# Kernel optimization log

Measured on AMD Instinct MI355X. Metric: run time of the kernel, lower is better.

## Reference

```python
import jax, jax.numpy as jnp
import numpy as np

D_MODEL = 1024
NUM_HEADS = 16
D_K = D_MODEL // NUM_HEADS
THETA = 10000.0
BATCH, SEQ = 2, 2048


def apply_rope(x, token_positions, theta):
    # x: [..., heads, seq, d_k]; interleaved pair rotation
    d = x.shape[-1]
    inv_freq = theta ** (-jnp.arange(0, d, 2, dtype=jnp.float32) / d)  # [d/2]
    ang = token_positions.astype(jnp.float32)[:, None] * inv_freq[None, :]  # [seq, d/2]
    cos, sin = jnp.cos(ang), jnp.sin(ang)  # broadcast over batch/heads
    x_even = x[..., 0::2]
    x_odd = x[..., 1::2]
    out_even = x_even * cos - x_odd * sin
    out_odd = x_even * sin + x_odd * cos
    out = jnp.stack([out_even, out_odd], axis=-1)  # [..., seq, d/2, 2]
    return out.reshape(x.shape)


def setup_inputs() -> dict:
    key = jax.random.key(0)
    ks = jax.random.split(key, 5)
    scale = 1.0 / np.sqrt(D_MODEL)
    return {
        "x": jax.random.normal(ks[0], (BATCH, SEQ, D_MODEL), dtype=jnp.float32),
        "wq": jax.random.normal(ks[1], (D_MODEL, D_MODEL), dtype=jnp.float32) * scale,
        "wk": jax.random.normal(ks[2], (D_MODEL, D_MODEL), dtype=jnp.float32) * scale,
        "wv": jax.random.normal(ks[3], (D_MODEL, D_MODEL), dtype=jnp.float32) * scale,
        "wo": jax.random.normal(ks[4], (D_MODEL, D_MODEL), dtype=jnp.float32) * scale,
        "token_positions": jnp.arange(SEQ, dtype=jnp.int32),
    }


def reference(x, wq, wk, wv, wo, token_positions):
    B, S, _ = x.shape
    # fused-style QKV projections: weight layout is [d_out, d_in]
    xq = jnp.einsum("bsd,kd->bsk", x, wq)
    xk = jnp.einsum("bsd,kd->bsk", x, wk)
    xv = jnp.einsum("bsd,vd->bsv", x, wv)
    # split heads: [b, h, s, d_h]
    def split(t):
        return t.reshape(B, S, NUM_HEADS, D_K).transpose(0, 2, 1, 3)
    xq, xk, xv = split(xq), split(xk), split(xv)
    xq = apply_rope(xq, token_positions, THETA)
    xk = apply_rope(xk, token_positions, THETA)
    scores = jnp.einsum("bhqd,bhkd->bhqk", xq, xk) / jnp.sqrt(jnp.float32(D_K))
    causal = jnp.tril(jnp.ones((S, S), dtype=bool))
    scores = jnp.where(causal, scores, -jnp.inf)
    attn = jax.nn.softmax(scores, axis=-1)
    out = jnp.einsum("bhqk,bhkd->bhqd", attn, xv)
    out = out.transpose(0, 2, 1, 3).reshape(B, S, D_MODEL)  # merge heads
    return jnp.einsum("bsv,dv->bsd", out, wo)
```

## Files before the change

kernel.cpp:

```cpp
#include <hip/hip_runtime.h>

typedef __attribute__((ext_vector_type(8))) short short8;
typedef __attribute__((ext_vector_type(4))) short short4v;
typedef __attribute__((ext_vector_type(4))) float floatx4;

__device__ inline ushort f2b(float f) {
    union { uint i; float f; } c; c.f = f;
    uint i = c.i;
    uint r = (i + 0x7FFFu + ((i >> 16) & 1u)) >> 16;
    return (ushort)r;
}

__device__ __forceinline__ void load_lds16(const ushort* g, ushort* l) {
    __builtin_amdgcn_global_load_lds((const __attribute__((address_space(1))) void*)g,
                                     (__attribute__((address_space(3))) void*)l, 16, 0, 0);
}

__global__ __launch_bounds__(256) void cvt4_k(const float* __restrict__ x,
                                              const float* __restrict__ wq,
                                              const float* __restrict__ wk,
                                              const float* __restrict__ wv,
                                              ushort* __restrict__ xb,
                                              ushort* __restrict__ wqb,
                                              ushort* __restrict__ wkb,
                                              ushort* __restrict__ wvb,
                                              const int* __restrict__ pos,
                                              float2* __restrict__ tab) {
    const int blk = blockIdx.x;
    if (blk >= 3584) {
        const int idx = (blk - 3584) * 256 + threadIdx.x;
        const int s = idx >> 5, fi = idx & 31;
        const float inv = exp2f(-(float)fi * 0.41524101186092557f);
        const float ang = (float)pos[s] * inv;
        float sn, cs;
        sincosf(ang, &sn, &cs);
        tab[idx] = make_float2(cs, sn);
        return;
    }
    const float* in; ushort* out; int base;
    if (blk < 2048)      { in = x;  out = xb;  base = blk; }
    else if (blk < 2560) { in = wq; out = wqb; base = blk - 2048; }
    else if (blk < 3072) { in = wk; out = wkb; base = blk - 2560; }
    else                 { in = wv; out = wvb; base = blk - 3072; }
    const int i = (base * 256 + threadIdx.x) * 8;
    float4 f0 = *(const float4*)(in + i);
    float4 f1 = *(const float4*)(in + i + 4);
    ushort u[8] = {f2b(f0.x), f2b(f0.y), f2b(f0.z), f2b(f0.w),
                   f2b(f1.x), f2b(f1.y), f2b(f1.z), f2b(f1.w)};
    *(uint4*)(out + i) = *(const uint4*)u;
}

__global__ __launch_bounds__(256) void cvt_k(const float* __restrict__ in,
                                             ushort* __restrict__ out, int n) {
    const int i = (blockIdx.x * 256 + threadIdx.x) * 8;
    if (i >= n) return;
    float4 f0 = *(const float4*)(in + i);
    float4 f1 = *(const float4*)(in + i + 4);
    ushort u[8] = {f2b(f0.x), f2b(f0.y), f2b(f0.z), f2b(f0.w),
                   f2b(f1.x), f2b(f1.y), f2b(f1.z), f2b(f1.w)};
    *(uint4*)(out + i) = *(const uint4*)u;
}

template <bool OUTF32>
__device__ __forceinline__ void gemm_body8(ushort* As, ushort* Bs,
                                           const ushort* __restrict__ A,
                                           const ushort* __restrict__ B,
                                           void* __restrict__ C,
                                           int N, int m0, int n0,
                                           bool doRope, const float2* __restrict__ tab,
                                           float oscale) {
    const int tid = threadIdx.x;
    const int wave = tid >> 6, lane = tid & 63;
    const int quad = lane >> 4, l16 = lane & 15;
    const int wm = (wave >> 2) * 64, wn = (wave & 3) * 32;

    floatx4 acc[4][2] = {};

    const int rA = tid >> 2, jgA = ((tid & 3) - (rA >> 1)) & 3;
    const ushort* ga = A + (size_t)(m0 + rA) * 1024 + jgA * 8;
    const ushort* gb = B + (size_t)(n0 + rA) * 1024 + jgA * 8;

    load_lds16(ga, As + tid * 8);
    load_lds16(gb, Bs + tid * 8);
    __syncthreads();

    for (int kt = 0; kt < 32; ++kt) {
        const int cur = kt & 1;
        if (kt + 1 < 32) {
            const int nb = (cur ^ 1) * 4096;
            load_lds16(ga + (kt + 1) * 32, As + nb + tid * 8);
            load_lds16(gb + (kt + 1) * 32, Bs + nb + tid * 8);
        }
        const ushort* as = As + cur * 4096;
        const ushort* bs = Bs + cur * 4096;
        short8 af[4], bf[2];
#pragma unroll
        for (int i = 0; i < 4; ++i) {
            const int ra = wm + i * 16 + l16;
            af[i] = *(const short8*)(as + ra * 32 + (((quad + (ra >> 1)) & 3) << 3));
        }
#pragma unroll
        for (int j = 0; j < 2; ++j) {
            const int rb = wn + j * 16 + l16;
            bf[j] = *(const short8*)(bs + rb * 32 + (((quad + (rb >> 1)) & 3) << 3));
        }
#pragma unroll
        for (int mi = 0; mi < 4; ++mi)
#pragma unroll
            for (int ni = 0; ni < 2; ++ni)
                acc[mi][ni] = __builtin_amdgcn_mfma_f32_16x16x32_bf16(af[mi], bf[ni], acc[mi][ni], 0, 0, 0);
        __syncthreads();
    }
#pragma unroll
    for (int mi = 0; mi < 4; ++mi) {
        const int row = m0 + wm + mi * 16 + quad * 4;
#pragma unroll
        for (int ni = 0; ni < 2; ++ni) {
            const int col = n0 + wn + ni * 16 + l16;
            const int fi = ((wn + ni * 16 + l16) & 63) >> 1;
#pragma unroll
            for (int r = 0; r < 4; ++r) {
                float v = acc[mi][ni][r];
                if (doRope) {
                    const float other = __shfl_xor(v, 1);
                    const float2 cs = tab[((row + r) & 2047) * 32 + fi];
                    v = (col & 1) ? (other * cs.y + v * cs.x) : (v * cs.x - other * cs.y);
                }
                v *= oscale;
                if (OUTF32) ((float*)C)[(size_t)(row + r) * N + col] = v;
                else        ((ushort*)C)[(size_t)(row + r) * N + col] = f2b(v);
            }
        }
    }
}

__global__ __launch_bounds__(512) void gemm_qkv(const ushort* __restrict__ xb,
                                                const ushort* __restrict__ wqb,
                                                const ushort* __restrict__ wkb,
                                                const ushort* __restrict__ wvb,
                                                ushort* __restrict__ q,
                                                ushort* __restrict__ k,
                                                ushort* __restrict__ vt,
                                                const float2* __restrict__ tab) {
    __shared__ __align__(16) ushort As[8192], Bs[8192];
    const int blk = blockIdx.x;
    const int job = blk >> 8, r = blk & 255;
    const ushort *A, *B;
    ushort* C;
    int N, m0, n0;
    bool rope;
    float osc;
    if (job == 0)      { A = xb;  B = wqb; C = q;  N = 1024; m0 = (r >> 3) * 128; n0 = (r & 7) * 128; rope = true;  osc = 0.18033688011112042f; }
    else if (job == 1) { A = xb;  B = wkb; C = k;  N = 1024; m0 = (r >> 3) * 128; n0 = (r & 7) * 128; rope = true;  osc = 1.0f; }
    else               { A = wvb; B = xb;  C = vt; N = 4096; m0 = (r & 7) * 128;  n0 = (r >> 3) * 128; rope = false; osc = 1.0f; }
    gemm_body8<false>(As, Bs, A, B, C, N, m0, n0, rope, tab, osc);
}

__global__ __launch_bounds__(512) void gemm_o(const ushort* __restrict__ A,
                                              const ushort* __restrict__ B,
                                              float* __restrict__ C) {
    __shared__ __align__(16) ushort As[8192];
    __shared__ __align__(16) ushort Bs[4096];

    const int blk = blockIdx.x;
    const int m0 = (blk >> 4) * 128, n0 = (blk & 15) * 64;

    const int tid = threadIdx.x;
    const int wave = tid >> 6, lane = tid & 63;
    const int quad = lane >> 4, l16 = lane & 15;
    const int wm = (wave >> 2) * 64, wn = (wave & 3) * 16;

    floatx4 acc[4] = {};

    const int rA = tid >> 2, jgA = ((tid & 3) - (rA >> 1)) & 3;
    const ushort* ga = A + (size_t)(m0 + rA) * 1024 + jgA * 8;
    const int rB = (tid & 255) >> 2, jgB = (((tid & 255) & 3) - (rB >> 1)) & 3;
    const ushort* gb = B + (size_t)(n0 + rB) * 1024 + jgB * 8;

    load_lds16(ga, As + tid * 8);
    if (tid < 256) load_lds16(gb, Bs + tid * 8);
    __syncthreads();

    for (int kt = 0; kt < 32; ++kt) {
        const int cur = kt & 1;
        if (kt + 1 < 32) {
            load_lds16(ga + (kt + 1) * 32, As + (cur ^ 1) * 4096 + tid * 8);
            if (tid < 256)
                load_lds16(gb + (kt + 1) * 32, Bs + (cur ^ 1) * 2048 + tid * 8);
        }
        const ushort* as = As + cur * 4096;
        const ushort* bs = Bs + cur * 2048;
        short8 af[4], bf;
#pragma unroll
        for (int i = 0; i < 4; ++i) {
            const int ra = wm + i * 16 + l16;
            af[i] = *(const short8*)(as + ra * 32 + (((quad + (ra >> 1)) & 3) << 3));
        }
        {
            const int rb = wn + l16;
            bf = *(const short8*)(bs + rb * 32 + (((quad + (rb >> 1)) & 3) << 3));
        }
#pragma unroll
        for (int mi = 0; mi < 4; ++mi)
            acc[mi] = __builtin_amdgcn_mfma_f32_16x16x32_bf16(af[mi], bf, acc[mi], 0, 0, 0);
        __syncthreads();
    }
#pragma unroll
    for (int mi = 0; mi < 4; ++mi) {
        const int row = m0 + wm + mi * 16 + quad * 4;
        const int col = n0 + wn + l16;
#pragma unroll
        for (int r = 0; r < 4; ++r)
            C[(size_t)(row + r) * 1024 + col] = acc[mi][r];
    }
}

__global__ __launch_bounds__(256, 4) void attn_k(const ushort* __restrict__ Qg,
                                                 const ushort* __restrict__ Kg,
                                                 const ushort* __restrict__ Vtg,
                                                 ushort* __restrict__ Og,
                                                 const float* __restrict__ wo,
                                                 ushort* __restrict__ wob) {
    __shared__ __align__(16) ushort Ks[2][4096];
    __shared__ __align__(16) ushort Vs[2][4096];

    const int tid = threadIdx.x;
    const int blk = blockIdx.x;
    if (blk >= 1024) {
        const int i = ((blk - 1024) * 256 + tid) * 8;
        float4 f0 = *(const float4*)(wo + i);
        float4 f1 = *(const float4*)(wo + i + 4);
        ushort u[8] = {f2b(f0.x), f2b(f0.y), f2b(f0.z), f2b(f0.w),
                       f2b(f1.x), f2b(f1.y), f2b(f1.z), f2b(f1.w)};
        *(uint4*)(wob + i) = *(const uint4*)u;
        return;
    }
    const int wave = tid >> 6, lane = tid & 63;
    const int quad = lane >> 4, l16 = lane & 15;
    const int g = blk >> 8, rem = blk & 255;
    const int t = rem >> 5, bh = rem & 31;
    int qt;
    if (g == 0)      qt = 31 - t;
    else if (g == 1) qt = 23 - t;
    else if (g == 2) qt = t;
    else             qt = 8 + t;
    const int b = bh >> 4, h = bh & 15;
    const int bq = b * 2048;
    const int wl = wave * 16 + l16;
    const int nk = qt + 1, dt = nk - 1;

    const int cA = tid, cB = tid + 256;
    const int sA = cA >> 3, jA = ((cA & 7) - sA) & 7;
    const int sB = cB >> 3, jB = ((cB & 7) - sB) & 7;
    const ushort* kgA = Kg + (size_t)(bq + sA) * 1024 + h * 64 + jA * 8;
    const ushort* kgB = Kg + (size_t)(bq + sB) * 1024 + h * 64 + jB * 8;
    const ushort* vgA = Vtg + (size_t)(h * 64 + sA) * 4096 + bq + jA * 8;
    const ushort* vgB = Vtg + (size_t)(h * 64 + sB) * 4096 + bq + jB * 8;

    const int kb0 = l16 * 64 + (((quad + l16) & 7) << 3);
    const int kb1 = l16 * 64 + (((quad + 4 + l16) & 7) << 3);
    int vbs[4];
#pragma unroll
    for (int cb = 0; cb < 4; ++cb)
        vbs[cb] = l16 * 64 + (((cb * 2 + (quad >> 1) + l16) & 7) << 3) + (quad & 1) * 4;

    const ushort* qrow = Qg + (size_t)(bq + qt * 64 + wl) * 1024 + h * 64 + quad * 8;
    const short8 qf0 = *(const short8*)qrow;
    const short8 qf1 = *(const short8*)(qrow + 32);

    floatx4 od[4] = {};
    float l_st = 0.0f;

    load_lds16(kgA, &Ks[0][cA * 8]);
    load_lds16(kgB, &Ks[0][cB * 8]);
    load_lds16(vgA, &Vs[0][cA * 8]);
    load_lds16(vgB, &Vs[0][cB * 8]);
    __syncthreads();

    const ushort* kgA2 = kgA + 65536;
    const ushort* kgB2 = kgB + 65536;
    const ushort* vgA2 = vgA + 64;
    const ushort* vgB2 = vgB + 64;

    auto step = [&](int kt, bool diag, bool pref) {
        const int cur = kt & 1;
        if (pref) {
            const int nxt = cur ^ 1;
            load_lds16(kgA2, &Ks[nxt][cA * 8]);
            load_lds16(kgB2, &Ks[nxt][cB * 8]);
            load_lds16(vgA2, &Vs[nxt][cA * 8]);
            load_lds16(vgB2, &Vs[nxt][cB * 8]);
            kgA2 += 65536; kgB2 += 65536; vgA2 += 64; vgB2 += 64;
        }
        const ushort* kc = &Ks[cur][0];
        const ushort* vc = &Vs[cur][0];

        floatx4 st[4];
        __builtin_amdgcn_s_setprio(1);
#pragma unroll
        for (int cb = 0; cb < 4; ++cb) {
            short8 kf0 = *(const short8*)(kc + kb0 + cb * 1024);
            short8 kf1 = *(const short8*)(kc + kb1 + cb * 1024);
            floatx4 z = {};
            z = __builtin_amdgcn_mfma_f32_16x16x32_bf16(kf0, qf0, z, 0, 0, 0);
            z = __builtin_amdgcn_mfma_f32_16x16x32_bf16(kf1, qf1, z, 0, 0, 0);
            st[cb] = z;
        }
        __builtin_amdgcn_s_setprio(0);

        float pv[4][4];
        float sum = 0.0f;
#pragma unroll
        for (int cb = 0; cb < 4; ++cb) {
            const int scb = cb * 16 + quad * 4;
#pragma unroll
            for (int r = 0; r < 4; ++r) {
                float e = __builtin_amdgcn_exp2f(st[cb][r]);
                if (diag && (scb + r > wl)) e = 0.0f;
                pv[cb][r] = e;
                sum += e;
            }
        }
        l_st += sum;

        short4v pb[4];
#pragma unroll
        for (int cb = 0; cb < 4; ++cb) {
            uint lo_, hi_;
            asm("v_cvt_pk_bf16_f32 %0, %1, %2" : "=v"(lo_) : "v"(pv[cb][0]), "v"(pv[cb][1]));
            asm("v_cvt_pk_bf16_f32 %0, %1, %2" : "=v"(hi_) : "v"(pv[cb][2]), "v"(pv[cb][3]));
            union { uint u[2]; short4v s; } cvu;
            cvu.u[0] = lo_; cvu.u[1] = hi_;
            pb[cb] = cvu.s;
        }

        __builtin_amdgcn_s_setprio(1);
#pragma unroll
        for (int db = 0; db < 4; ++db) {
#pragma unroll
            for (int cb = 0; cb < 4; ++cb) {
                short4v vf = *(const short4v*)(vc + vbs[cb] + db * 1024);
                od[db] = __builtin_amdgcn_mfma_f32_16x16x16bf16_1k(vf, pb[cb], od[db], 0, 0, 0);
            }
        }
        __builtin_amdgcn_s_setprio(0);
        if (pref) __syncthreads();
    };

    for (int kt = 0; kt < dt; ++kt) step(kt, false, true);
    step(dt, true, false);

    l_st += __shfl_xor(l_st, 16);
    l_st += __shfl_xor(l_st, 32);

    const float linv = 1.0f / l_st;
    ushort* orow = Og + (size_t)(bq + qt * 64 + wl) * 1024 + h * 64 + quad * 4;
#pragma unroll
    for (int db = 0; db < 4; ++db) {
        uint2 w;
        w.x = (uint)f2b(od[db][0] * linv) | ((uint)f2b(od[db][1] * linv) << 16);
        w.y = (uint)f2b(od[db][2] * linv) | ((uint)f2b(od[db][3] * linv) << 16);
        *(uint2*)(orow + db * 16) = w;
    }
}

extern "C" void kernel_launch(void* const* d_in, const int* in_sizes, int n_in,
                              void* d_out, int out_size, void* d_ws, size_t ws_size,
                              hipStream_t stream) {
    const float* x  = (const float*)d_in[0];
    const float* wq = (const float*)d_in[1];
    const float* wk = (const float*)d_in[2];
    const float* wv = (const float*)d_in[3];
    const float* wo = (const float*)d_in[4];
    const int* pos  = (const int*)d_in[5];

    const size_t NX = (size_t)4096 * 1024;
    const size_t NW = (size_t)1024 * 1024;

    ushort* q_ws  = (ushort*)d_ws;
    ushort* k_ws  = q_ws + NX;
    ushort* vt_ws = k_ws + NX;
    ushort* o_ws  = vt_ws + NX;
    ushort* xb  = (ushort*)d_out;
    ushort* wqb = xb + NX;
    ushort* wkb = wqb + NW;
    ushort* wvb = wkb + NW;
    float2* tab = (float2*)(wvb + NW);

    const bool merged = ws_size >= (4 * NX + NW) * sizeof(ushort);
    ushort* wob = merged ? (o_ws + NX) : q_ws;

    cvt4_k<<<dim3(3840), 256, 0, stream>>>(x, wq, wk, wv, xb, wqb, wkb, wvb, pos, tab);
    gemm_qkv<<<dim3(768), 512, 0, stream>>>(xb, wqb, wkb, wvb, q_ws, k_ws, vt_ws, tab);
    attn_k<<<dim3(merged ? 1536 : 1024), 256, 0, stream>>>(q_ws, k_ws, vt_ws, o_ws, wo, wob);
    if (!merged)
        cvt_k<<<dim3(512), 256, 0, stream>>>(wo, q_ws, (int)NW);
    gemm_o<<<dim3(512), 512, 0, stream>>>(o_ws, wob, (float*)d_out);
}
```

Baseline: 179.4 us.

## Pair complementary causal query tiles in one 512-thread attention block sharing K/V loads

The attention kernel now packs two query tiles into one 8-wave block: one half takes a late tile (qt=31-j) and the other an early tile (qt=j). Both halves share the same staged K/V tiles in LDS, so the early tile's K/V loads are reused and every block does balanced causal work. The cost is that half the waves sit idle (still hitting barriers) once the short tile finishes, and there are fewer, larger blocks with different occupancy.

```diff
diff --git a/kernel.cpp b/kernel.cpp
--- a/kernel.cpp
+++ b/kernel.cpp
@@ -215,7 +215,7 @@
     }
 }
 
-__global__ __launch_bounds__(256, 4) void attn_k(const ushort* __restrict__ Qg,
+__global__ __launch_bounds__(512, 4) void attn_k(const ushort* __restrict__ Qg,
                                                  const ushort* __restrict__ Kg,
                                                  const ushort* __restrict__ Vtg,
                                                  ushort* __restrict__ Og,
@@ -226,8 +226,8 @@
 
     const int tid = threadIdx.x;
     const int blk = blockIdx.x;
-    if (blk >= 1024) {
-        const int i = ((blk - 1024) * 256 + tid) * 8;
+    if (blk >= 512) {
+        const int i = ((blk - 512) * 512 + tid) * 8;
         float4 f0 = *(const float4*)(wo + i);
         float4 f1 = *(const float4*)(wo + i + 4);
         ushort u[8] = {f2b(f0.x), f2b(f0.y), f2b(f0.z), f2b(f0.w),
@@ -237,25 +237,21 @@
     }
     const int wave = tid >> 6, lane = tid & 63;
     const int quad = lane >> 4, l16 = lane & 15;
-    const int g = blk >> 8, rem = blk & 255;
-    const int t = rem >> 5, bh = rem & 31;
-    int qt;
-    if (g == 0)      qt = 31 - t;
-    else if (g == 1) qt = 23 - t;
-    else if (g == 2) qt = t;
-    else             qt = 8 + t;
+    const int half = wave >> 2, wv = wave & 3;
+    const int bh = blk & 31;
+    const int t = blk >> 5;
+    const int jIdx = (t < 8) ? t : (23 - t);
+    const int qt = half ? jIdx : (31 - jIdx);
+    const int nkA = 32 - jIdx;
+    const int nkB = jIdx + 1;
+    const int nk = half ? nkB : nkA;
     const int b = bh >> 4, h = bh & 15;
     const int bq = b * 2048;
-    const int wl = wave * 16 + l16;
-    const int nk = qt + 1, dt = nk - 1;
-
-    const int cA = tid, cB = tid + 256;
-    const int sA = cA >> 3, jA = ((cA & 7) - sA) & 7;
-    const int sB = cB >> 3, jB = ((cB & 7) - sB) & 7;
-    const ushort* kgA = Kg + (size_t)(bq + sA) * 1024 + h * 64 + jA * 8;
-    const ushort* kgB = Kg + (size_t)(bq + sB) * 1024 + h * 64 + jB * 8;
-    const ushort* vgA = Vtg + (size_t)(h * 64 + sA) * 4096 + bq + jA * 8;
-    const ushort* vgB = Vtg + (size_t)(h * 64 + sB) * 4096 + bq + jB * 8;
+    const int wl = wv * 16 + l16;
+
+    const int sK = tid >> 3, jK = ((tid & 7) - sK) & 7;
+    const ushort* kg = Kg + (size_t)(bq + sK) * 1024 + h * 64 + jK * 8;
+    const ushort* vg = Vtg + (size_t)(h * 64 + sK) * 4096 + bq + jK * 8;
 
     const int kb0 = l16 * 64 + (((quad + l16) & 7) << 3);
     const int kb1 = l16 * 64 + (((quad + 4 + l16) & 7) << 3);
@@ -271,84 +267,79 @@
     floatx4 od[4] = {};
     float l_st = 0.0f;
 
-    load_lds16(kgA, &Ks[0][cA * 8]);
-    load_lds16(kgB, &Ks[0][cB * 8]);
-    load_lds16(vgA, &Vs[0][cA * 8]);
-    load_lds16(vgB, &Vs[0][cB * 8]);
+    load_lds16(kg, &Ks[0][tid * 8]);
+    load_lds16(vg, &Vs[0][tid * 8]);
     __syncthreads();
 
-    const ushort* kgA2 = kgA + 65536;
-    const ushort* kgB2 = kgB + 65536;
-    const ushort* vgA2 = vgA + 64;
-    const ushort* vgB2 = vgB + 64;
-
-    auto step = [&](int kt, bool diag, bool pref) {
+    const ushort* kg2 = kg + 65536;
+    const ushort* vg2 = vg + 64;
+
+    for (int kt = 0; kt < nkA; ++kt) {
         const int cur = kt & 1;
+        const bool pref = (kt + 1 < nkA);
         if (pref) {
             const int nxt = cur ^ 1;
-            load_lds16(kgA2, &Ks[nxt][cA * 8]);
-            load_lds16(kgB2, &Ks[nxt][cB * 8]);
-            load_lds16(vgA2, &Vs[nxt][cA * 8]);
-            load_lds16(vgB2, &Vs[nxt][cB * 8]);
-            kgA2 += 65536; kgB2 += 65536; vgA2 += 64; vgB2 += 64;
-        }
-        const ushort* kc = &Ks[cur][0];
-        const ushort* vc = &Vs[cur][0];
-
-        floatx4 st[4];
-        __builtin_amdgcn_s_setprio(1);
-#pragma unroll
-        for (int cb = 0; cb < 4; ++cb) {
-            short8 kf0 = *(const short8*)(kc + kb0 + cb * 1024);
-            short8 kf1 = *(const short8*)(kc + kb1 + cb * 1024);
-            floatx4 z = {};
-            z = __builtin_amdgcn_mfma_f32_16x16x32_bf16(kf0, qf0, z, 0, 0, 0);
-            z = __builtin_amdgcn_mfma_f32_16x16x32_bf16(kf1, qf1, z, 0, 0, 0);
-            st[cb] = z;
-        }
-        __builtin_amdgcn_s_setprio(0);
-
-        float pv[4][4];
-        float sum = 0.0f;
-#pragma unroll
-        for (int cb = 0; cb < 4; ++cb) {
-            const int scb = cb * 16 + quad * 4;
-#pragma unroll
-            for (int r = 0; r < 4; ++r) {
-                float e = __builtin_amdgcn_exp2f(st[cb][r]);
-                if (diag && (scb + r > wl)) e = 0.0f;
-                pv[cb][r] = e;
-                sum += e;
-            }
-        }
-        l_st += sum;
-
-        short4v pb[4];
-#pragma unroll
-        for (int cb = 0; cb < 4; ++cb) {
-            uint lo_, hi_;
-            asm("v_cvt_pk_bf16_f32 %0, %1, %2" : "=v"(lo_) : "v"(pv[cb][0]), "v"(pv[cb][1]));
-            asm("v_cvt_pk_bf16_f32 %0, %1, %2" : "=v"(hi_) : "v"(pv[cb][2]), "v"(pv[cb][3]));
-            union { uint u[2]; short4v s; } cvu;
-            cvu.u[0] = lo_; cvu.u[1] = hi_;
-            pb[cb] = cvu.s;
-        }
-
-        __builtin_amdgcn_s_setprio(1);
-#pragma unroll
-        for (int db = 0; db < 4; ++db) {
+            load_lds16(kg2, &Ks[nxt][tid * 8]);
+            load_lds16(vg2, &Vs[nxt][tid * 8]);
+            kg2 += 65536; vg2 += 64;
+        }
+        if (!half || kt < nkB) {
+            const bool diag = (kt == nk - 1);
+            const ushort* kc = &Ks[cur][0];
+            const ushort* vc = &Vs[cur][0];
+
+            floatx4 st[4];
+            __builtin_amdgcn_s_setprio(1);
 #pragma unroll
             for (int cb = 0; cb < 4; ++cb) {
-                short4v vf = *(const short4v*)(vc + vbs[cb] + db * 1024);
-                od[db] = __builtin_amdgcn_mfma_f32_16x16x16bf16_1k(vf, pb[cb], od[db], 0, 0, 0);
-            }
-        }
-        __builtin_amdgcn_s_setprio(0);
+                short8 kf0 = *(const short8*)(kc + kb0 + cb * 1024);
+                short8 kf1 = *(const short8*)(kc + kb1 + cb * 1024);
+                floatx4 z = {};
+                z = __builtin_amdgcn_mfma_f32_16x16x32_bf16(kf0, qf0, z, 0, 0, 0);
+                z = __builtin_amdgcn_mfma_f32_16x16x32_bf16(kf1, qf1, z, 0, 0, 0);
+                st[cb] = z;
+            }
+            __builtin_amdgcn_s_setprio(0);
+
+            float pv[4][4];
+            float sum = 0.0f;
+#pragma unroll
+            for (int cb = 0; cb < 4; ++cb) {
+                const int scb = cb * 16 + quad * 4;
+#pragma unroll
+                for (int r = 0; r < 4; ++r) {
+                    float e = __builtin_amdgcn_exp2f(st[cb][r]);
+                    if (diag && (scb + r > wl)) e = 0.0f;
+                    pv[cb][r] = e;
+                    sum += e;
+                }
+            }
+            l_st += sum;
+
+            short4v pb[4];
+#pragma unroll
+            for (int cb = 0; cb < 4; ++cb) {
+                uint lo_, hi_;
+                asm("v_cvt_pk_bf16_f32 %0, %1, %2" : "=v"(lo_) : "v"(pv[cb][0]), "v"(pv[cb][1]));
+                asm("v_cvt_pk_bf16_f32 %0, %1, %2" : "=v"(hi_) : "v"(pv[cb][2]), "v"(pv[cb][3]));
+                union { uint u[2]; short4v s; } cvu;
+                cvu.u[0] = lo_; cvu.u[1] = hi_;
+                pb[cb] = cvu.s;
+            }
+
+            __builtin_amdgcn_s_setprio(1);
+#pragma unroll
+            for (int db = 0; db < 4; ++db) {
+#pragma unroll
+                for (int cb = 0; cb < 4; ++cb) {
+                    short4v vf = *(const short4v*)(vc + vbs[cb] + db * 1024);
+                    od[db] = __builtin_amdgcn_mfma_f32_16x16x16bf16_1k(vf, pb[cb], od[db], 0, 0, 0);
+                }
+            }
+            __builtin_amdgcn_s_setprio(0);
+        }
         if (pref) __syncthreads();
-    };
-
-    for (int kt = 0; kt < dt; ++kt) step(kt, false, true);
-    step(dt, true, false);
+    }
 
     l_st += __shfl_xor(l_st, 16);
     l_st += __shfl_xor(l_st, 32);
@@ -392,7 +383,7 @@
 
     cvt4_k<<<dim3(3840), 256, 0, stream>>>(x, wq, wk, wv, xb, wqb, wkb, wvb, pos, tab);
     gemm_qkv<<<dim3(768), 512, 0, stream>>>(xb, wqb, wkb, wvb, q_ws, k_ws, vt_ws, tab);
-    attn_k<<<dim3(merged ? 1536 : 1024), 256, 0, stream>>>(q_ws, k_ws, vt_ws, o_ws, wo, wob);
+    attn_k<<<dim3(merged ? 768 : 512), 512, 0, stream>>>(q_ws, k_ws, vt_ws, o_ws, wo, wob);
     if (!merged)
         cvt_k<<<dim3(512), 256, 0, stream>>>(wo, q_ws, (int)NW);
     gemm_o<<<dim3(512), 512, 0, stream>>>(o_ws, wob, (float*)d_out);
```

Result: no change. 178.0 us (-0.8%).
